# Kernel tuning notes

Measured on AMD Instinct MI355X. Metric: run time of the kernel, lower is better.

Reference implementation:

```python
import jax, jax.numpy as jnp
import numpy as np

N_NODES = 50000
N_EDGES = 800000
HIDDEN = 128


def setup_inputs() -> dict:
    key = jax.random.key(0)
    ks = jax.random.split(key, 8)
    node_feat = jax.random.normal(ks[0], (N_NODES, HIDDEN), dtype=jnp.float32)
    edge_feat = jax.random.normal(ks[1], (N_EDGES, HIDDEN), dtype=jnp.float32)
    edge_src = jax.random.randint(ks[2], (N_EDGES,), 0, N_NODES, dtype=jnp.int32)
    edge_dst = jax.random.randint(ks[3], (N_EDGES,), 0, N_NODES, dtype=jnp.int32)
    # MLP params: Linear(h, 2h) -> ReLU -> Linear(2h, h); Kaiming-ish scale
    w1 = jax.random.normal(ks[4], (HIDDEN, 2 * HIDDEN), dtype=jnp.float32) * (1.0 / np.sqrt(HIDDEN))
    b1 = jnp.zeros((2 * HIDDEN,), dtype=jnp.float32)
    w2 = jax.random.normal(ks[5], (2 * HIDDEN, HIDDEN), dtype=jnp.float32) * (1.0 / np.sqrt(2 * HIDDEN))
    b2 = jnp.zeros((HIDDEN,), dtype=jnp.float32)
    return {"node_feat": node_feat, "edge_feat": edge_feat,
            "edge_src": edge_src, "edge_dst": edge_dst,
            "w1": w1, "b1": b1, "w2": w2, "b2": b2}


def reference(node_feat, edge_feat, edge_src, edge_dst, w1, b1, w2, b2):
    # Message: gather src node features per edge, add edge features
    msg = node_feat[edge_src] + edge_feat                     # [E, H]
    # Reduce: scatter-sum messages into destination nodes
    agg = jax.ops.segment_sum(msg, edge_dst, num_segments=node_feat.shape[0])  # [N, H]
    # 2-layer MLP with ReLU
    h = jax.nn.relu(agg @ w1 + b1)                            # [N, 2H]
    out = h @ w2 + b2                                         # [N, H]
    return out
```

## Files before the change

### kernel.cpp

```cpp
#include <hip/hip_runtime.h>


constexpr int NN  = 50000;
constexpr int NE  = 800000;
constexpr int H   = 128;
constexpr int H2  = 256;
constexpr int SHP = 264;
constexpr int CAP = 64;

typedef short short8_t __attribute__((ext_vector_type(8)));
typedef float f32x4    __attribute__((ext_vector_type(4)));
typedef int   i32x4    __attribute__((ext_vector_type(4)));

__device__ inline short f2bf(float f) {
    union { float f; unsigned u; } c; c.f = f;
    unsigned r = c.u + 0x7FFF + ((c.u >> 16) & 1);
    return (short)(r >> 16);
}

__device__ inline f32x4 nt4(const float* p) {
    return __builtin_nontemporal_load((const f32x4*)p);
}

__global__ __launch_bounds__(256) void pack_zero_kernel(
    const float* __restrict__ w1, const float* __restrict__ w2,
    short* __restrict__ w1p, short* __restrict__ w2p,
    int* __restrict__ cursor)
{
    int i = blockIdx.x * 256 + threadIdx.x;
    {
        int j = i & 7, l = (i >> 3) & 63, ct = (i >> 9) & 15, kk = i >> 13;
        w1p[i] = f2bf(w1[(kk * 32 + (l >> 4) * 8 + j) * H2 + ct * 16 + (l & 15)]);
    }
    {
        int j = i & 7, l = (i >> 3) & 63, ct = (i >> 9) & 7, kk = i >> 12;
        w2p[i] = f2bf(w2[(kk * 32 + (l >> 4) * 8 + j) * H + ct * 16 + (l & 15)]);
    }
    if (i < NN) cursor[i] = 0;
    const int i2 = i + 32768;
    if (i2 < NN) cursor[i2] = 0;
}

__global__ __launch_bounds__(256) void place_kernel(
    const int* __restrict__ edge_dst, const int* __restrict__ edge_src,
    int* __restrict__ cursor, int2* __restrict__ bucket)
{
    const int e0 = (blockIdx.x * blockDim.x + threadIdx.x) * 2;
    if (e0 + 1 < NE) {
        const int2 d = *(const int2*)&edge_dst[e0];
        const int2 s = *(const int2*)&edge_src[e0];
        const int p0 = atomicAdd(&cursor[d.x], 1);
        bucket[(size_t)d.x * CAP + p0] = make_int2(e0, s.x);
        const int p1 = atomicAdd(&cursor[d.y], 1);
        bucket[(size_t)d.y * CAP + p1] = make_int2(e0 + 1, s.y);
    } else if (e0 < NE) {
        const int d = edge_dst[e0];
        const int s = edge_src[e0];
        const int p = atomicAdd(&cursor[d], 1);
        bucket[(size_t)d * CAP + p] = make_int2(e0, s);
    }
}

__global__ __launch_bounds__(256) void gather_kernel(
    const float* __restrict__ node_feat,
    const float* __restrict__ edge_feat,
    const int2*  __restrict__ bucket,
    const int*   __restrict__ cursor,
    short*       __restrict__ aggb)
{
    const int node = blockIdx.x * 4 + (threadIdx.x >> 6);
    const int lane = threadIdx.x & 63;
    const int h    = lane >> 5;
    const int c4   = (lane & 31) * 4;
    const int deg  = cursor[node];
    const int2* bk = bucket + (size_t)node * CAP;
    f32x4 acc = {0.f, 0.f, 0.f, 0.f};

    const int ng = deg >> 2;
    i32x4 c0 = {0, 0, 0, 0}, c1 = {0, 0, 0, 0};
    if (ng > 0) {
        c0 = *(const i32x4*)&bk[0];
        c1 = *(const i32x4*)&bk[2];
    }
    int i = 0;
    for (int g = 0; g < ng; ++g) {
        const i32x4 q0 = c0, q1 = c1;
        if (g + 1 < ng) {
            c0 = *(const i32x4*)&bk[i + 4];
            c1 = *(const i32x4*)&bk[i + 6];
        }
        const int e0 = h ? q0.z : q0.x, s0 = h ? q0.w : q0.y;
        const int e1 = h ? q1.z : q1.x, s1 = h ? q1.w : q1.y;
        const f32x4 a0 = nt4(edge_feat + (size_t)e0 * H + c4);
        const f32x4 b0 = *(const f32x4*)(node_feat + (size_t)s0 * H + c4);
        const f32x4 a1 = nt4(edge_feat + (size_t)e1 * H + c4);
        const f32x4 b1 = *(const f32x4*)(node_feat + (size_t)s1 * H + c4);
        acc += a0 + b0;
        acc += a1 + b1;
        i += 4;
    }
    if (i + 2 <= deg) {
        const i32x4 p0 = *(const i32x4*)&bk[i];
        const int e0 = h ? p0.z : p0.x, s0 = h ? p0.w : p0.y;
        const f32x4 a0 = nt4(edge_feat + (size_t)e0 * H + c4);
        const f32x4 b0 = *(const f32x4*)(node_feat + (size_t)s0 * H + c4);
        acc += a0 + b0;
        i += 2;
    }
    if (i < deg && h == 0) {
        const int2 es = bk[i];
        const f32x4 ef = nt4(edge_feat + (size_t)es.x * H + c4);
        const f32x4 nf = *(const f32x4*)(node_feat + (size_t)es.y * H + c4);
        acc += ef + nf;
    }

    acc.x += __shfl_xor(acc.x, 32);
    acc.y += __shfl_xor(acc.y, 32);
    acc.z += __shfl_xor(acc.z, 32);
    acc.w += __shfl_xor(acc.w, 32);

    if (h == 0) {
        const unsigned lo = (unsigned)(unsigned short)f2bf(acc.x)
                          | ((unsigned)(unsigned short)f2bf(acc.y) << 16);
        const unsigned hi = (unsigned)(unsigned short)f2bf(acc.z)
                          | ((unsigned)(unsigned short)f2bf(acc.w) << 16);
        *(uint2*)(aggb + (size_t)node * H + c4) = make_uint2(lo, hi);
    }
}

__global__ __launch_bounds__(256) void mlp_kernel(
    const short* __restrict__ aggb, const short* __restrict__ w1p,
    const short* __restrict__ w2p,  const float* __restrict__ b1,
    const float* __restrict__ b2,   float* __restrict__ out)
{
    __shared__ short smem[4 * 16 * SHP];
    const int t = threadIdx.x;
    const int wid = t >> 6, l = t & 63;
    const int lrow = l & 15, lk = l >> 4;
    const long long mrow = (long long)blockIdx.x * 64 + wid * 16;
    short* s_h = &smem[wid * 16 * SHP];

    f32x4 acc[16];
    #pragma unroll
    for (int ct = 0; ct < 16; ++ct) acc[ct] = (f32x4){0.f, 0.f, 0.f, 0.f};
    const short8_t* bfr1 = (const short8_t*)w1p;
    #pragma unroll
    for (int kk = 0; kk < 4; ++kk) {
        short8_t a = {0, 0, 0, 0, 0, 0, 0, 0};
        if (mrow + lrow < NN)
            a = *(const short8_t*)(aggb + (mrow + lrow) * H + kk * 32 + lk * 8);
        #pragma unroll
        for (int ct = 0; ct < 16; ++ct)
            acc[ct] = __builtin_amdgcn_mfma_f32_16x16x32_bf16(
                a, bfr1[(kk * 16 + ct) * 64 + l], acc[ct], 0, 0, 0);
    }
    #pragma unroll
    for (int ct = 0; ct < 16; ++ct) {
        const float b = b1[ct * 16 + lrow];
        #pragma unroll
        for (int r = 0; r < 4; ++r) {
            float v = acc[ct][r] + b;
            s_h[(lk * 4 + r) * SHP + ct * 16 + lrow] = f2bf(v > 0.f ? v : 0.f);
        }
    }
    __syncthreads();

    f32x4 acc2[8];
    #pragma unroll
    for (int ct = 0; ct < 8; ++ct) acc2[ct] = (f32x4){0.f, 0.f, 0.f, 0.f};
    const short8_t* bfr2 = (const short8_t*)w2p;
    #pragma unroll
    for (int kk = 0; kk < 8; ++kk) {
        const short8_t a = *(const short8_t*)&s_h[lrow * SHP + kk * 32 + lk * 8];
        #pragma unroll
        for (int ct = 0; ct < 8; ++ct)
            acc2[ct] = __builtin_amdgcn_mfma_f32_16x16x32_bf16(
                a, bfr2[(kk * 8 + ct) * 64 + l], acc2[ct], 0, 0, 0);
    }
    __syncthreads();

    float* sc = (float*)s_h;
    #pragma unroll
    for (int ct = 0; ct < 8; ++ct) {
        const float b = b2[ct * 16 + lrow];
        #pragma unroll
        for (int r = 0; r < 4; ++r)
            sc[(lk * 4 + r) * 132 + ct * 16 + lrow] = acc2[ct][r] + b;
    }
    __syncthreads();

    #pragma unroll
    for (int it = 0; it < 8; ++it) {
        const int off = it * 64 + l;
        const long long row = mrow + (off >> 5);
        if (row < NN) {
            const float4 v = *(const float4*)&sc[(off >> 5) * 132 + (off & 31) * 4];
            *(float4*)(out + row * H + (off & 31) * 4) = v;
        }
    }
}

__global__ __launch_bounds__(256) void scatter_kernel(
    const float* __restrict__ node_feat,
    const float* __restrict__ edge_feat,
    const int*   __restrict__ edge_src,
    const int*   __restrict__ edge_dst,
    float*       __restrict__ agg)
{
    long long tid = (long long)blockIdx.x * blockDim.x + threadIdx.x;
    const long long total = (long long)NE * 32;
    if (tid >= total) return;
    int e = (int)(tid >> 5);
    int q = (int)((tid & 31) << 2);
    int s = edge_src[e];
    int d = edge_dst[e];
    const float4 nf = *(const float4*)(node_feat + (long long)s * H + q);
    const float4 ef = *(const float4*)(edge_feat + (long long)e * H + q);
    float* dst = agg + (long long)d * H + q;
    atomicAdd(dst + 0, nf.x + ef.x);
    atomicAdd(dst + 1, nf.y + ef.y);
    atomicAdd(dst + 2, nf.z + ef.z);
    atomicAdd(dst + 3, nf.w + ef.w);
}

__global__ __launch_bounds__(256) void mlp_simple_kernel(
    const float* __restrict__ agg,
    const float* __restrict__ w1, const float* __restrict__ b1,
    const float* __restrict__ w2, const float* __restrict__ b2,
    float*       __restrict__ out)
{
    constexpr int NPB = 16;
    __shared__ float s_in[NPB][H];
    __shared__ float s_h [NPB][H2];
    const int t = threadIdx.x;
    const long long base = (long long)blockIdx.x * NPB;
    {
        const float4* src = (const float4*)(agg + base * H);
        float4* dst = (float4*)(&s_in[0][0]);
        dst[t]       = src[t];
        dst[t + 256] = src[t + 256];
    }
    __syncthreads();
    float acc[NPB];
    {
        const float b = b1[t];
        #pragma unroll
        for (int n = 0; n < NPB; ++n) acc[n] = b;
    }
    #pragma unroll 4
    for (int k = 0; k < H; ++k) {
        const float w = w1[k * H2 + t];
        #pragma unroll
        for (int n = 0; n < NPB; ++n) acc[n] = fmaf(s_in[n][k], w, acc[n]);
    }
    #pragma unroll
    for (int n = 0; n < NPB; ++n) s_h[n][t] = fmaxf(acc[n], 0.0f);
    __syncthreads();
    const int j = t & (H - 1);
    const int g = t >> 7;
    float acc2[NPB / 2];
    {
        const float b = b2[j];
        #pragma unroll
        for (int n = 0; n < NPB / 2; ++n) acc2[n] = b;
    }
    #pragma unroll 4
    for (int k = 0; k < H2; ++k) {
        const float w = w2[k * H + j];
        #pragma unroll
        for (int n = 0; n < NPB / 2; ++n)
            acc2[n] = fmaf(s_h[g * (NPB / 2) + n][k], w, acc2[n]);
    }
    #pragma unroll
    for (int n = 0; n < NPB / 2; ++n)
        out[(base + g * (NPB / 2) + n) * H + j] = acc2[n];
}

__global__ __launch_bounds__(256) void zero_agg_kernel(float4* __restrict__ p, int n4)
{
    int i = blockIdx.x * blockDim.x + threadIdx.x;
    if (i < n4) p[i] = make_float4(0.f, 0.f, 0.f, 0.f);
}

extern "C" void kernel_launch(void* const* d_in, const int* in_sizes, int n_in,
                              void* d_out, int out_size, void* d_ws, size_t ws_size,
                              hipStream_t stream)
{
    const float* node_feat = (const float*)d_in[0];
    const float* edge_feat = (const float*)d_in[1];
    const int*   edge_src  = (const int*)  d_in[2];
    const int*   edge_dst  = (const int*)  d_in[3];
    const float* w1 = (const float*)d_in[4];
    const float* b1 = (const float*)d_in[5];
    const float* w2 = (const float*)d_in[6];
    const float* b2 = (const float*)d_in[7];
    float* out = (float*)d_out;

    const size_t cursor_b = ((size_t)NN * 4 + 255) & ~(size_t)255;
    const size_t w1p_b    = (size_t)32768 * 2;
    const size_t w2p_b    = (size_t)32768 * 2;
    const size_t bucket_b = (size_t)NN * CAP * 8;
    const size_t aggb_b   = ((size_t)NN * H * 2 + 255) & ~(size_t)255;
    const size_t need     = cursor_b + w1p_b + w2p_b + bucket_b + aggb_b;

    if (ws_size >= need) {
        char* p = (char*)d_ws;
        int*   cursor = (int*)p;                 p += cursor_b;
        short* w1p    = (short*)p;               p += w1p_b;
        short* w2p    = (short*)p;               p += w2p_b;
        int2*  bucket = (int2*)p;                p += bucket_b;
        short* aggb   = (short*)p;

        pack_zero_kernel<<<128, 256, 0, stream>>>(w1, w2, w1p, w2p, cursor);
        const int eb = 256;
        const int eg = (NE / 2 + eb - 1) / eb;
        place_kernel<<<eg, eb, 0, stream>>>(edge_dst, edge_src, cursor, bucket);
        gather_kernel<<<NN / 4, 256, 0, stream>>>(
            node_feat, edge_feat, bucket, cursor, aggb);
        const int mlp_grid = (NN + 63) / 64;
        mlp_kernel<<<mlp_grid, 256, 0, stream>>>(aggb, w1p, w2p, b1, b2, out);
    } else {
        const size_t agg_bytes = (size_t)NN * H * sizeof(float);
        float* agg = (ws_size >= agg_bytes) ? (float*)d_ws : out;
        {
            const int n4 = (int)(agg_bytes / 16);
            zero_agg_kernel<<<(n4 + 255) / 256, 256, 0, stream>>>((float4*)agg, n4);
        }
        const long long total = (long long)NE * 32;
        const int block = 256;
        const int grid  = (int)((total + block - 1) / block);
        scatter_kernel<<<grid, block, 0, stream>>>(
            node_feat, edge_feat, edge_src, edge_dst, agg);
        mlp_simple_kernel<<<NN / 16, 256, 0, stream>>>(agg, w1, b1, w2, b2, out);
    }
}
```

Measured before the change: 219.9 us.

## Fuse edge gather-reduce into MLP kernel via shared-memory staging

Merges the per-node gather/segment-sum kernel into the MLP kernel. Each block aggregates 64 nodes into an LDS tile of bf16 features, then runs the MFMA MLP directly from LDS. This drops the global bf16 intermediate buffer and one kernel launch. In exchange, each wave processes 16 nodes serially, the grid is much smaller and LDS use rises, which may reduce the memory parallelism available to the gather.

```diff
diff --git a/kernel.cpp b/kernel.cpp
--- a/kernel.cpp
+++ b/kernel.cpp
@@ -6,6 +6,7 @@
 constexpr int H   = 128;
 constexpr int H2  = 256;
 constexpr int SHP = 264;
+constexpr int SIN = 136;
 constexpr int CAP = 64;
 
 typedef short short8_t __attribute__((ext_vector_type(8)));
@@ -61,83 +62,83 @@
     }
 }
 
-__global__ __launch_bounds__(256) void gather_kernel(
+__global__ __launch_bounds__(256) void fused_kernel(
     const float* __restrict__ node_feat,
     const float* __restrict__ edge_feat,
     const int2*  __restrict__ bucket,
     const int*   __restrict__ cursor,
-    short*       __restrict__ aggb)
-{
-    const int node = blockIdx.x * 4 + (threadIdx.x >> 6);
-    const int lane = threadIdx.x & 63;
-    const int h    = lane >> 5;
-    const int c4   = (lane & 31) * 4;
-    const int deg  = cursor[node];
-    const int2* bk = bucket + (size_t)node * CAP;
-    f32x4 acc = {0.f, 0.f, 0.f, 0.f};
-
-    const int ng = deg >> 2;
-    i32x4 c0 = {0, 0, 0, 0}, c1 = {0, 0, 0, 0};
-    if (ng > 0) {
-        c0 = *(const i32x4*)&bk[0];
-        c1 = *(const i32x4*)&bk[2];
-    }
-    int i = 0;
-    for (int g = 0; g < ng; ++g) {
-        const i32x4 q0 = c0, q1 = c1;
-        if (g + 1 < ng) {
-            c0 = *(const i32x4*)&bk[i + 4];
-            c1 = *(const i32x4*)&bk[i + 6];
-        }
-        const int e0 = h ? q0.z : q0.x, s0 = h ? q0.w : q0.y;
-        const int e1 = h ? q1.z : q1.x, s1 = h ? q1.w : q1.y;
-        const f32x4 a0 = nt4(edge_feat + (size_t)e0 * H + c4);
-        const f32x4 b0 = *(const f32x4*)(node_feat + (size_t)s0 * H + c4);
-        const f32x4 a1 = nt4(edge_feat + (size_t)e1 * H + c4);
-        const f32x4 b1 = *(const f32x4*)(node_feat + (size_t)s1 * H + c4);
-        acc += a0 + b0;
-        acc += a1 + b1;
-        i += 4;
-    }
-    if (i + 2 <= deg) {
-        const i32x4 p0 = *(const i32x4*)&bk[i];
-        const int e0 = h ? p0.z : p0.x, s0 = h ? p0.w : p0.y;
-        const f32x4 a0 = nt4(edge_feat + (size_t)e0 * H + c4);
-        const f32x4 b0 = *(const f32x4*)(node_feat + (size_t)s0 * H + c4);
-        acc += a0 + b0;
-        i += 2;
-    }
-    if (i < deg && h == 0) {
-        const int2 es = bk[i];
-        const f32x4 ef = nt4(edge_feat + (size_t)es.x * H + c4);
-        const f32x4 nf = *(const f32x4*)(node_feat + (size_t)es.y * H + c4);
-        acc += ef + nf;
-    }
-
-    acc.x += __shfl_xor(acc.x, 32);
-    acc.y += __shfl_xor(acc.y, 32);
-    acc.z += __shfl_xor(acc.z, 32);
-    acc.w += __shfl_xor(acc.w, 32);
-
-    if (h == 0) {
-        const unsigned lo = (unsigned)(unsigned short)f2bf(acc.x)
-                          | ((unsigned)(unsigned short)f2bf(acc.y) << 16);
-        const unsigned hi = (unsigned)(unsigned short)f2bf(acc.z)
-                          | ((unsigned)(unsigned short)f2bf(acc.w) << 16);
-        *(uint2*)(aggb + (size_t)node * H + c4) = make_uint2(lo, hi);
-    }
-}
-
-__global__ __launch_bounds__(256) void mlp_kernel(
-    const short* __restrict__ aggb, const short* __restrict__ w1p,
-    const short* __restrict__ w2p,  const float* __restrict__ b1,
-    const float* __restrict__ b2,   float* __restrict__ out)
-{
+    const short* __restrict__ w1p, const short* __restrict__ w2p,
+    const float* __restrict__ b1,  const float* __restrict__ b2,
+    float*       __restrict__ out)
+{
+    __shared__ short s_in[64 * SIN];
     __shared__ short smem[4 * 16 * SHP];
+
     const int t = threadIdx.x;
     const int wid = t >> 6, l = t & 63;
+    const int h   = l >> 5;
+    const int c4  = (l & 31) * 4;
+    const long long nbase = (long long)blockIdx.x * 64;
+
+    for (int nl = 0; nl < 16; ++nl) {
+        const int lrow_n = wid * 16 + nl;
+        const long long node = nbase + lrow_n;
+        const int deg = (node < NN) ? cursor[node] : 0;
+        const int2* bk = bucket + (size_t)node * CAP;
+        f32x4 acc = {0.f, 0.f, 0.f, 0.f};
+        int i = 0;
+        const int ng = deg >> 2;
+        i32x4 c0 = {0, 0, 0, 0}, c1 = {0, 0, 0, 0};
+        if (ng > 0) {
+            c0 = *(const i32x4*)&bk[0];
+            c1 = *(const i32x4*)&bk[2];
+        }
+        for (int g = 0; g < ng; ++g) {
+            const i32x4 q0 = c0, q1 = c1;
+            if (g + 1 < ng) {
+                c0 = *(const i32x4*)&bk[i + 4];
+                c1 = *(const i32x4*)&bk[i + 6];
+            }
+            const int e0 = h ? q0.z : q0.x, s0 = h ? q0.w : q0.y;
+            const int e1 = h ? q1.z : q1.x, s1 = h ? q1.w : q1.y;
+            const f32x4 a0 = nt4(edge_feat + (size_t)e0 * H + c4);
+            const f32x4 b0 = *(const f32x4*)(node_feat + (size_t)s0 * H + c4);
+            const f32x4 a1 = nt4(edge_feat + (size_t)e1 * H + c4);
+            const f32x4 b1v = *(const f32x4*)(node_feat + (size_t)s1 * H + c4);
+            acc += a0 + b0;
+            acc += a1 + b1v;
+            i += 4;
+        }
+        if (i + 2 <= deg) {
+            const i32x4 p0 = *(const i32x4*)&bk[i];
+            const int e0 = h ? p0.z : p0.x, s0 = h ? p0.w : p0.y;
+            const f32x4 a0 = nt4(edge_feat + (size_t)e0 * H + c4);
+            const f32x4 b0 = *(const f32x4*)(node_feat + (size_t)s0 * H + c4);
+            acc += a0 + b0;
+            i += 2;
+        }
+        if (i < deg && h == 0) {
+            const int2 es = bk[i];
+            const f32x4 ef = nt4(edge_feat + (size_t)es.x * H + c4);
+            const f32x4 nf = *(const f32x4*)(node_feat + (size_t)es.y * H + c4);
+            acc += ef + nf;
+        }
+        acc.x += __shfl_xor(acc.x, 32);
+        acc.y += __shfl_xor(acc.y, 32);
+        acc.z += __shfl_xor(acc.z, 32);
+        acc.w += __shfl_xor(acc.w, 32);
+        if (h == 0) {
+            const unsigned lo = (unsigned)(unsigned short)f2bf(acc.x)
+                              | ((unsigned)(unsigned short)f2bf(acc.y) << 16);
+            const unsigned hi = (unsigned)(unsigned short)f2bf(acc.z)
+                              | ((unsigned)(unsigned short)f2bf(acc.w) << 16);
+            *(uint2*)&s_in[lrow_n * SIN + c4] = make_uint2(lo, hi);
+        }
+    }
+    __syncthreads();
+
     const int lrow = l & 15, lk = l >> 4;
-    const long long mrow = (long long)blockIdx.x * 64 + wid * 16;
+    const long long mrow = nbase + wid * 16;
     short* s_h = &smem[wid * 16 * SHP];
 
     f32x4 acc[16];
@@ -146,9 +147,8 @@
     const short8_t* bfr1 = (const short8_t*)w1p;
     #pragma unroll
     for (int kk = 0; kk < 4; ++kk) {
-        short8_t a = {0, 0, 0, 0, 0, 0, 0, 0};
-        if (mrow + lrow < NN)
-            a = *(const short8_t*)(aggb + (mrow + lrow) * H + kk * 32 + lk * 8);
+        const short8_t a =
+            *(const short8_t*)&s_in[(wid * 16 + lrow) * SIN + kk * 32 + lk * 8];
         #pragma unroll
         for (int ct = 0; ct < 16; ++ct)
             acc[ct] = __builtin_amdgcn_mfma_f32_16x16x32_bf16(
@@ -300,25 +300,22 @@
     const size_t w1p_b    = (size_t)32768 * 2;
     const size_t w2p_b    = (size_t)32768 * 2;
     const size_t bucket_b = (size_t)NN * CAP * 8;
-    const size_t aggb_b   = ((size_t)NN * H * 2 + 255) & ~(size_t)255;
-    const size_t need     = cursor_b + w1p_b + w2p_b + bucket_b + aggb_b;
+    const size_t need     = cursor_b + w1p_b + w2p_b + bucket_b;
 
     if (ws_size >= need) {
         char* p = (char*)d_ws;
         int*   cursor = (int*)p;                 p += cursor_b;
         short* w1p    = (short*)p;               p += w1p_b;
         short* w2p    = (short*)p;               p += w2p_b;
-        int2*  bucket = (int2*)p;                p += bucket_b;
-        short* aggb   = (short*)p;
+        int2*  bucket = (int2*)p;
 
         pack_zero_kernel<<<128, 256, 0, stream>>>(w1, w2, w1p, w2p, cursor);
         const int eb = 256;
         const int eg = (NE / 2 + eb - 1) / eb;
         place_kernel<<<eg, eb, 0, stream>>>(edge_dst, edge_src, cursor, bucket);
-        gather_kernel<<<NN / 4, 256, 0, stream>>>(
-            node_feat, edge_feat, bucket, cursor, aggb);
-        const int mlp_grid = (NN + 63) / 64;
-        mlp_kernel<<<mlp_grid, 256, 0, stream>>>(aggb, w1p, w2p, b1, b2, out);
+        const int fgrid = (NN + 63) / 64;
+        fused_kernel<<<fgrid, 256, 0, stream>>>(
+            node_feat, edge_feat, bucket, cursor, w1p, w2p, b1, b2, out);
     } else {
         const size_t agg_bytes = (size_t)NN * H * sizeof(float);
         float* agg = (ws_size >= agg_bytes) ? (float*)d_ws : out;
```

After: 288.9 us. 1.31x slower.
